# Performance work log

Measured on AMD Instinct MI355X. Metric: run time of the kernel, lower is better.

Reference implementation:

```python
import jax, jax.numpy as jnp
import numpy as np

H = 8
LN_EPS = 1e-5


def _layer_norm(t):
    # LayerNorm over last dim, no affine (elementwise_affine=False, bias=False)
    mu = jnp.mean(t, axis=-1, keepdims=True)
    var = jnp.var(t, axis=-1, keepdims=True)
    return (t - mu) / jnp.sqrt(var + LN_EPS)


def setup_inputs() -> dict:
    key = jax.random.key(0)
    ks = jax.random.split(key, 7)
    B, N, D, K = 2, 8192, 512, 32
    x = jax.random.normal(ks[0], (B, N, D), dtype=jnp.float32)
    idx = jax.random.randint(ks[1], (N, K), 0, N)
    s = 1.0 / np.sqrt(D)  # kaiming-ish init scale for stability
    Wq = jax.random.normal(ks[2], (D, D), dtype=jnp.float32) * s
    Wk = jax.random.normal(ks[3], (D, D), dtype=jnp.float32) * s
    Wv = jax.random.normal(ks[4], (D, D), dtype=jnp.float32) * s
    Wout = jax.random.normal(ks[5], (D, D), dtype=jnp.float32) * s
    bout = jnp.zeros((D,), dtype=jnp.float32)
    return {"x": x, "idx": idx, "Wq": Wq, "Wk": Wk, "Wv": Wv, "Wout": Wout, "bout": bout}


def reference(x, idx, Wq, Wk, Wv, Wout, bout):
    B, N, D = x.shape
    d_k = D // H

    def proj(W):
        # torch Linear: x @ W.T ; reshape to (B, H, N, d_k)
        return (x @ W.T).reshape(B, N, H, d_k).transpose(0, 2, 1, 3)

    Q, K, V = proj(Wq), proj(Wk), proj(Wv)
    # per-head LayerNorm on d_k (all heads identical since no affine params)
    Q = _layer_norm(Q)
    K = _layer_norm(K)

    # grouped (neighborhood) attention: gather K,V at neighbor indices
    Kg = K[:, :, idx]  # (B, H, N, k, d_k)
    Vg = V[:, :, idx]  # (B, H, N, k, d_k)
    scores = jnp.einsum('bhnd,bhnkd->bhnk', Q, Kg) / jnp.sqrt(jnp.asarray(d_k, x.dtype))
    attn = jax.nn.softmax(scores, axis=-1)
    out = jnp.einsum('bhnk,bhnkd->bhnd', attn, Vg)  # (B, H, N, d_k)

    out = out.transpose(0, 2, 1, 3).reshape(B, N, D)
    return out @ Wout.T + bout
```

## Files before the change

### kernel.cpp

```cpp
#include <hip/hip_runtime.h>
#include <hip/hip_bf16.h>
#include <math.h>

#define BB 2
#define NN 8192
#define DD 512
#define HH 8
#define DK 64
#define KNB 32
#define BN (BB*NN)
#define BHN (BB*HH*NN)

typedef __attribute__((ext_vector_type(8))) short bf16x8;
typedef __attribute__((ext_vector_type(8))) unsigned short us8;
typedef __attribute__((ext_vector_type(4))) float f32x4;

__device__ __forceinline__ float bf2f(unsigned short u) {
    return __uint_as_float(((unsigned)u) << 16);
}
__device__ __forceinline__ unsigned short f2bf(float f) {
    return __bfloat16_as_ushort(__float2bfloat16(f));
}

__device__ __forceinline__ void gload_lds16(const void* gptr, void* lptr) {
    __builtin_amdgcn_global_load_lds(
        (const __attribute__((address_space(1))) unsigned int*)gptr,
        (__attribute__((address_space(3))) unsigned int*)lptr,
        16, 0, 0);
}

__global__ __launch_bounds__(256) void cvt_x(const float* __restrict__ in,
                                             unsigned short* __restrict__ out) {
    const int i = (blockIdx.x * 256 + threadIdx.x) * 4;
    const float4 v = *(const float4*)(in + i);
    ushort4 u;
    u.x = f2bf(v.x); u.y = f2bf(v.y); u.z = f2bf(v.z); u.w = f2bf(v.w);
    *(ushort4*)(out + i) = u;
}

__global__ __launch_bounds__(256) void cvt_w(const float* __restrict__ Wq, const float* __restrict__ Wk,
                                             const float* __restrict__ Wv, const float* __restrict__ Wo,
                                             unsigned short* __restrict__ Wfb,
                                             unsigned short* __restrict__ Wob) {
    const int e = (blockIdx.x * 256 + threadIdx.x) * 4;
    const int t = e >> 18;
    const int off = e & 262143;
    const float* src = (t == 0) ? Wq : (t == 1) ? Wk : (t == 2) ? Wv : Wo;
    unsigned short* dst = (t < 3) ? (Wfb + (size_t)t * 262144) : Wob;
    const float4 v = *(const float4*)(src + off);
    ushort4 u;
    u.x = f2bf(v.x); u.y = f2bf(v.y); u.z = f2bf(v.z); u.w = f2bf(v.w);
    *(ushort4*)(dst + off) = u;
}

__global__ __launch_bounds__(256) void gemm_qkv(
    const unsigned short* __restrict__ Xb, const unsigned short* __restrict__ Wfb,
    unsigned short* __restrict__ Qh, unsigned short* __restrict__ Kh,
    unsigned short* __restrict__ Vh)
{
    __shared__ unsigned short Als[128 * 32];
    __shared__ unsigned short Bls[128 * 32];
    const int tid  = threadIdx.x;
    const int wave = tid >> 6, lane = tid & 63;
    const int wm = wave >> 1, wn = wave & 1;
    const int quad = lane >> 4, r = lane & 15;
    const int row0 = blockIdx.x * 128;
    const int c0   = blockIdx.y * 128;

    f32x4 acc[4][4];
    #pragma unroll
    for (int i = 0; i < 4; ++i)
        #pragma unroll
        for (int j = 0; j < 4; ++j) acc[i][j] = (f32x4)0.f;

    const char* Ab = (const char*)Xb;
    const char* Bb = (const char*)Wfb;

    for (int k0 = 0; k0 < 512; k0 += 32) {
        __syncthreads();
        #pragma unroll
        for (int q = 0; q < 2; ++q) {
            const int li = q * 4096 + wave * 1024 + lane * 16;
            const int rr = li >> 6, off = li & 63;
            gload_lds16(Ab + (size_t)(row0 + rr) * 1024 + k0 * 2 + off,
                        (char*)Als + (q * 4096 + wave * 1024));
            gload_lds16(Bb + (size_t)(c0 + rr) * 1024 + k0 * 2 + off,
                        (char*)Bls + (q * 4096 + wave * 1024));
        }
        __syncthreads();

        bf16x8 af[4], bf[4];
        #pragma unroll
        for (int i = 0; i < 4; ++i)
            af[i] = *(const bf16x8*)(&Als[(wm * 64 + i * 16 + r) * 32 + quad * 8]);
        #pragma unroll
        for (int j = 0; j < 4; ++j)
            bf[j] = *(const bf16x8*)(&Bls[(wn * 64 + j * 16 + r) * 32 + quad * 8]);
        #pragma unroll
        for (int i = 0; i < 4; ++i)
            #pragma unroll
            for (int j = 0; j < 4; ++j)
                acc[i][j] = __builtin_amdgcn_mfma_f32_16x16x32_bf16(af[i], bf[j], acc[i][j], 0, 0, 0);
    }

    const int tensor = c0 >> 9;
    unsigned short* OutH = (tensor == 0) ? Qh : (tensor == 1) ? Kh : Vh;

    float mu[4][4], rs[4][4];
    if (tensor < 2) {
        #pragma unroll
        for (int i = 0; i < 4; ++i) {
            #pragma unroll
            for (int reg = 0; reg < 4; ++reg) {
                float sm = acc[i][0][reg] + acc[i][1][reg] + acc[i][2][reg] + acc[i][3][reg];
                sm += __shfl_xor(sm, 1); sm += __shfl_xor(sm, 2);
                sm += __shfl_xor(sm, 4); sm += __shfl_xor(sm, 8);
                const float muv = sm * (1.f / 64.f);
                float qv = 0.f;
                #pragma unroll
                for (int j = 0; j < 4; ++j) {
                    const float dv = acc[i][j][reg] - muv;
                    qv = fmaf(dv, dv, qv);
                }
                qv += __shfl_xor(qv, 1); qv += __shfl_xor(qv, 2);
                qv += __shfl_xor(qv, 4); qv += __shfl_xor(qv, 8);
                mu[i][reg] = muv;
                rs[i][reg] = rsqrtf(qv * (1.f / 64.f) + 1e-5f);
            }
        }
    }

    #pragma unroll
    for (int i = 0; i < 4; ++i) {
        #pragma unroll
        for (int j = 0; j < 4; ++j) {
            const int cc = (c0 & 511) + wn * 64 + j * 16 + r;
            const int h = cc >> 6, d = cc & 63;
            #pragma unroll
            for (int reg = 0; reg < 4; ++reg) {
                const int row = row0 + wm * 64 + i * 16 + quad * 4 + reg;
                const int b = row >> 13, n = row & 8191;
                float v = acc[i][j][reg];
                if (tensor < 2) v = (v - mu[i][reg]) * rs[i][reg];
                OutH[(((size_t)(b * HH + h) * NN + n) << 6) + d] = f2bf(v);
            }
        }
    }
}

__global__ __launch_bounds__(256) void attn(
    const unsigned short* __restrict__ Qh, const unsigned short* __restrict__ Kh,
    const unsigned short* __restrict__ Vh,
    const int* __restrict__ idx, unsigned short* __restrict__ Ob)
{
    const int p = blockIdx.x;
    const int L = ((p & 7) << 12) | (p >> 3);
    const int wid  = L * 4 + (threadIdx.x >> 6);
    const int lane = threadIdx.x & 63;
    const int bh = wid >> 13;
    const int n  = wid & 8191;
    const size_t base = (size_t)bh * NN * DK;

    const int k    = lane >> 1;
    const int half = lane & 1;
    const int g    = idx[n * KNB + k];

    const us8* q8 = (const us8*)(Qh + base + ((size_t)n << 6) + half * 32);
    const us8* k8 = (const us8*)(Kh + base + ((size_t)g << 6) + half * 32);
    float acc = 0.f;
    #pragma unroll
    for (int c = 0; c < 4; ++c) {
        const us8 qa = q8[c], ka = k8[c];
        #pragma unroll
        for (int e = 0; e < 8; ++e)
            acc = fmaf(bf2f(qa[e]), bf2f(ka[e]), acc);
    }
    float s = (acc + __shfl_xor(acc, 1)) * 0.125f;

    float m = s;
    #pragma unroll
    for (int off = 2; off <= 32; off <<= 1) m = fmaxf(m, __shfl_xor(m, off));
    const float e = __expf(s - m);
    float tot = e;
    #pragma unroll
    for (int off = 2; off <= 32; off <<= 1) tot += __shfl_xor(tot, off);
    const float pr = e / tot;

    float o = 0.f;
    #pragma unroll
    for (int kk = 0; kk < 32; ++kk) {
        const int   gk = __builtin_amdgcn_readlane(g, kk * 2);
        const float pk = __uint_as_float(
            __builtin_amdgcn_readlane(__float_as_uint(pr), kk * 2));
        o = fmaf(pk, bf2f(Vh[base + ((size_t)gk << 6) + lane]), o);
    }
    const int b = bh >> 3, h = bh & 7;
    Ob[((size_t)(b * NN + n)) * DD + h * DK + lane] = f2bf(o);
}

__global__ __launch_bounds__(256) void gemm_out(
    const unsigned short* __restrict__ Ob, const unsigned short* __restrict__ Wob,
    const float* __restrict__ bout, float* __restrict__ out)
{
    __shared__ unsigned short Als[128 * 32];
    __shared__ unsigned short Bls[128 * 32];
    const int tid  = threadIdx.x;
    const int wave = tid >> 6, lane = tid & 63;
    const int wm = wave >> 1, wn = wave & 1;
    const int quad = lane >> 4, r = lane & 15;
    const int row0 = blockIdx.x * 128;
    const int c0   = blockIdx.y * 128;

    f32x4 acc[4][4];
    #pragma unroll
    for (int i = 0; i < 4; ++i)
        #pragma unroll
        for (int j = 0; j < 4; ++j) acc[i][j] = (f32x4)0.f;

    const char* Ab = (const char*)Ob;
    const char* Bb = (const char*)Wob;

    for (int k0 = 0; k0 < 512; k0 += 32) {
        __syncthreads();
        #pragma unroll
        for (int q = 0; q < 2; ++q) {
            const int li = q * 4096 + wave * 1024 + lane * 16;
            const int rr = li >> 6, off = li & 63;
            gload_lds16(Ab + (size_t)(row0 + rr) * 1024 + k0 * 2 + off,
                        (char*)Als + (q * 4096 + wave * 1024));
            gload_lds16(Bb + (size_t)(c0 + rr) * 1024 + k0 * 2 + off,
                        (char*)Bls + (q * 4096 + wave * 1024));
        }
        __syncthreads();

        bf16x8 af[4], bf[4];
        #pragma unroll
        for (int i = 0; i < 4; ++i)
            af[i] = *(const bf16x8*)(&Als[(wm * 64 + i * 16 + r) * 32 + quad * 8]);
        #pragma unroll
        for (int j = 0; j < 4; ++j)
            bf[j] = *(const bf16x8*)(&Bls[(wn * 64 + j * 16 + r) * 32 + quad * 8]);
        #pragma unroll
        for (int i = 0; i < 4; ++i)
            #pragma unroll
            for (int j = 0; j < 4; ++j)
                acc[i][j] = __builtin_amdgcn_mfma_f32_16x16x32_bf16(af[i], bf[j], acc[i][j], 0, 0, 0);
    }

    #pragma unroll
    for (int i = 0; i < 4; ++i) {
        #pragma unroll
        for (int j = 0; j < 4; ++j) {
            const int colg = c0 + wn * 64 + j * 16 + r;
            const float bb = bout[colg];
            #pragma unroll
            for (int reg = 0; reg < 4; ++reg) {
                const int row = row0 + wm * 64 + i * 16 + quad * 4 + reg;
                out[((size_t)row << 9) + colg] = acc[i][j][reg] + bb;
            }
        }
    }
}

extern "C" void kernel_launch(void* const* d_in, const int* in_sizes, int n_in,
                              void* d_out, int out_size, void* d_ws, size_t ws_size,
                              hipStream_t stream)
{
    const float* x    = (const float*)d_in[0];
    const int*   idx  = (const int*)  d_in[1];
    const float* Wq   = (const float*)d_in[2];
    const float* Wk   = (const float*)d_in[3];
    const float* Wv   = (const float*)d_in[4];
    const float* Wout = (const float*)d_in[5];
    const float* bout = (const float*)d_in[6];

    char* ws = (char*)d_ws;
    unsigned short* Qh  = (unsigned short*)(ws);
    unsigned short* Kh  = (unsigned short*)(ws + 16777216);
    unsigned short* Vh  = (unsigned short*)(ws + 33554432);
    unsigned short* Xb  = (unsigned short*)(ws + 50331648);
    unsigned short* Ob  = Xb;
    unsigned short* Wfb = (unsigned short*)(ws + 67108864);
    unsigned short* Wob = (unsigned short*)(ws + 68681728);
    float* out = (float*)d_out;

    cvt_x<<<8192, 256, 0, stream>>>(x, Xb);
    cvt_w<<<1024, 256, 0, stream>>>(Wq, Wk, Wv, Wout, Wfb, Wob);

    dim3 g1(BN / 128, 1536 / 128);
    gemm_qkv<<<g1, 256, 0, stream>>>(Xb, Wfb, Qh, Kh, Vh);

    attn<<<BHN / 4, 256, 0, stream>>>(Qh, Kh, Vh, idx, Ob);

    dim3 g2(BN / 128, 512 / 128);
    gemm_out<<<g2, 256, 0, stream>>>(Ob, Wob, bout, out);
}
```

Before: 233.8 us.

## Switch pipeline from bf16 to fp16 with packed dot2 attention and merged conversion

Changes all intermediate storage and MFMA operations from bf16 to fp16. The attention kernel now uses packed fp16 dot2 instructions for the QK dot product and pairs two neighbors per step in the PV accumulation, halving the readlane and FMA work. The two conversion kernels are merged into one launch to save launch overhead. fp16 has a narrower range than bf16, so unnormalized V or x values risk overflow, and probabilities are rounded to fp16.

New measurement: 229.5 us. Within noise of the previous version (-1.8%).

```diff
diff --git a/kernel.cpp b/kernel.cpp
--- a/kernel.cpp
+++ b/kernel.cpp
@@ -11,15 +11,33 @@
 #define BN (BB*NN)
 #define BHN (BB*HH*NN)
 
-typedef __attribute__((ext_vector_type(8))) short bf16x8;
-typedef __attribute__((ext_vector_type(8))) unsigned short us8;
+typedef __attribute__((ext_vector_type(8))) _Float16 f16x8;
+typedef __attribute__((ext_vector_type(2))) _Float16 f16x2;
 typedef __attribute__((ext_vector_type(4))) float f32x4;
 
-__device__ __forceinline__ float bf2f(unsigned short u) {
-    return __uint_as_float(((unsigned)u) << 16);
-}
-__device__ __forceinline__ unsigned short f2bf(float f) {
-    return __bfloat16_as_ushort(__float2bfloat16(f));
+#if __has_builtin(__builtin_amdgcn_fdot2)
+#define HAS_FDOT2 1
+#endif
+
+__device__ __forceinline__ unsigned short f2h(float f) {
+    return __builtin_bit_cast(unsigned short, (_Float16)f);
+}
+__device__ __forceinline__ f16x2 u2h2(unsigned u) {
+    return __builtin_bit_cast(f16x2, u);
+}
+__device__ __forceinline__ float h2f_lo(unsigned u) {
+    return (float)__builtin_bit_cast(_Float16, (unsigned short)(u & 0xffffu));
+}
+__device__ __forceinline__ float h2f_hi(unsigned u) {
+    return (float)__builtin_bit_cast(_Float16, (unsigned short)(u >> 16));
+}
+__device__ __forceinline__ float dot2h(unsigned a, unsigned b, float c) {
+#ifdef HAS_FDOT2
+    return __builtin_amdgcn_fdot2(u2h2(a), u2h2(b), c, false);
+#else
+    c = fmaf(h2f_lo(a), h2f_lo(b), c);
+    return fmaf(h2f_hi(a), h2f_hi(b), c);
+#endif
 }
 
 __device__ __forceinline__ void gload_lds16(const void* gptr, void* lptr) {
@@ -29,27 +47,30 @@
         16, 0, 0);
 }
 
-__global__ __launch_bounds__(256) void cvt_x(const float* __restrict__ in,
-                                             unsigned short* __restrict__ out) {
-    const int i = (blockIdx.x * 256 + threadIdx.x) * 4;
-    const float4 v = *(const float4*)(in + i);
-    ushort4 u;
-    u.x = f2bf(v.x); u.y = f2bf(v.y); u.z = f2bf(v.z); u.w = f2bf(v.w);
-    *(ushort4*)(out + i) = u;
-}
-
-__global__ __launch_bounds__(256) void cvt_w(const float* __restrict__ Wq, const float* __restrict__ Wk,
-                                             const float* __restrict__ Wv, const float* __restrict__ Wo,
-                                             unsigned short* __restrict__ Wfb,
-                                             unsigned short* __restrict__ Wob) {
-    const int e = (blockIdx.x * 256 + threadIdx.x) * 4;
-    const int t = e >> 18;
-    const int off = e & 262143;
-    const float* src = (t == 0) ? Wq : (t == 1) ? Wk : (t == 2) ? Wv : Wo;
-    unsigned short* dst = (t < 3) ? (Wfb + (size_t)t * 262144) : Wob;
+__global__ __launch_bounds__(256) void cvt_all(
+    const float* __restrict__ x,
+    const float* __restrict__ Wq, const float* __restrict__ Wk,
+    const float* __restrict__ Wv, const float* __restrict__ Wo,
+    unsigned short* __restrict__ Xb, unsigned short* __restrict__ Wfb,
+    unsigned short* __restrict__ Wob)
+{
+    const int blk = blockIdx.x;
+    const float* src;
+    unsigned short* dst;
+    int off;
+    if (blk < 8192) {
+        off = (blk * 256 + threadIdx.x) * 4;
+        src = x; dst = Xb;
+    } else {
+        const int e = ((blk - 8192) * 256 + threadIdx.x) * 4;
+        const int t = e >> 18;
+        off = e & 262143;
+        src = (t == 0) ? Wq : (t == 1) ? Wk : (t == 2) ? Wv : Wo;
+        dst = (t < 3) ? (Wfb + (size_t)t * 262144) : Wob;
+    }
     const float4 v = *(const float4*)(src + off);
     ushort4 u;
-    u.x = f2bf(v.x); u.y = f2bf(v.y); u.z = f2bf(v.z); u.w = f2bf(v.w);
+    u.x = f2h(v.x); u.y = f2h(v.y); u.z = f2h(v.z); u.w = f2h(v.w);
     *(ushort4*)(dst + off) = u;
 }
 
@@ -89,18 +110,18 @@
         }
         __syncthreads();
 
-        bf16x8 af[4], bf[4];
+        f16x8 af[4], bf[4];
         #pragma unroll
         for (int i = 0; i < 4; ++i)
-            af[i] = *(const bf16x8*)(&Als[(wm * 64 + i * 16 + r) * 32 + quad * 8]);
+            af[i] = *(const f16x8*)(&Als[(wm * 64 + i * 16 + r) * 32 + quad * 8]);
         #pragma unroll
         for (int j = 0; j < 4; ++j)
-            bf[j] = *(const bf16x8*)(&Bls[(wn * 64 + j * 16 + r) * 32 + quad * 8]);
+            bf[j] = *(const f16x8*)(&Bls[(wn * 64 + j * 16 + r) * 32 + quad * 8]);
         #pragma unroll
         for (int i = 0; i < 4; ++i)
             #pragma unroll
             for (int j = 0; j < 4; ++j)
-                acc[i][j] = __builtin_amdgcn_mfma_f32_16x16x32_bf16(af[i], bf[j], acc[i][j], 0, 0, 0);
+                acc[i][j] = __builtin_amdgcn_mfma_f32_16x16x32_f16(af[i], bf[j], acc[i][j], 0, 0, 0);
     }
 
     const int tensor = c0 >> 9;
@@ -142,7 +163,7 @@
                 const int b = row >> 13, n = row & 8191;
                 float v = acc[i][j][reg];
                 if (tensor < 2) v = (v - mu[i][reg]) * rs[i][reg];
-                OutH[(((size_t)(b * HH + h) * NN + n) << 6) + d] = f2bf(v);
+                OutH[(((size_t)(b * HH + h) * NN + n) << 6) + d] = f2h(v);
             }
         }
     }
@@ -165,15 +186,16 @@
     const int half = lane & 1;
     const int g    = idx[n * KNB + k];
 
-    const us8* q8 = (const us8*)(Qh + base + ((size_t)n << 6) + half * 32);
-    const us8* k8 = (const us8*)(Kh + base + ((size_t)g << 6) + half * 32);
+    const uint4* q4 = (const uint4*)(Qh + base + ((size_t)n << 6) + half * 32);
+    const uint4* k4 = (const uint4*)(Kh + base + ((size_t)g << 6) + half * 32);
     float acc = 0.f;
     #pragma unroll
     for (int c = 0; c < 4; ++c) {
-        const us8 qa = q8[c], ka = k8[c];
-        #pragma unroll
-        for (int e = 0; e < 8; ++e)
-            acc = fmaf(bf2f(qa[e]), bf2f(ka[e]), acc);
+        const uint4 qa = q4[c], ka = k4[c];
+        acc = dot2h(qa.x, ka.x, acc);
+        acc = dot2h(qa.y, ka.y, acc);
+        acc = dot2h(qa.z, ka.z, acc);
+        acc = dot2h(qa.w, ka.w, acc);
     }
     float s = (acc + __shfl_xor(acc, 1)) * 0.125f;
 
@@ -186,16 +208,22 @@
     for (int off = 2; off <= 32; off <<= 1) tot += __shfl_xor(tot, off);
     const float pr = e / tot;
 
+    const unsigned prh = (unsigned)f2h(pr);
+    const unsigned pp = prh | (((unsigned)__shfl_xor((int)prh, 2)) << 16);
+    const unsigned gg = (unsigned)g | (((unsigned)__shfl_xor(g, 2)) << 16);
+
     float o = 0.f;
     #pragma unroll
-    for (int kk = 0; kk < 32; ++kk) {
-        const int   gk = __builtin_amdgcn_readlane(g, kk * 2);
-        const float pk = __uint_as_float(
-            __builtin_amdgcn_readlane(__float_as_uint(pr), kk * 2));
-        o = fmaf(pk, bf2f(Vh[base + ((size_t)gk << 6) + lane]), o);
+    for (int j = 0; j < 16; ++j) {
+        const unsigned gpair = (unsigned)__builtin_amdgcn_readlane((int)gg, j * 4);
+        const unsigned ppair = (unsigned)__builtin_amdgcn_readlane((int)pp, j * 4);
+        const int g0 = (int)(gpair & 0xffffu), g1 = (int)(gpair >> 16);
+        const unsigned v0 = Vh[base + ((size_t)g0 << 6) + lane];
+        const unsigned v1 = Vh[base + ((size_t)g1 << 6) + lane];
+        o = dot2h(v0 | (v1 << 16), ppair, o);
     }
     const int b = bh >> 3, h = bh & 7;
-    Ob[((size_t)(b * NN + n)) * DD + h * DK + lane] = f2bf(o);
+    Ob[((size_t)(b * NN + n)) * DD + h * DK + lane] = f2h(o);
 }
 
 __global__ __launch_bounds__(256) void gemm_out(
@@ -233,18 +261,18 @@
         }
         __syncthreads();
 
-        bf16x8 af[4], bf[4];
+        f16x8 af[4], bf[4];
         #pragma unroll
         for (int i = 0; i < 4; ++i)
-            af[i] = *(const bf16x8*)(&Als[(wm * 64 + i * 16 + r) * 32 + quad * 8]);
+            af[i] = *(const f16x8*)(&Als[(wm * 64 + i * 16 + r) * 32 + quad * 8]);
         #pragma unroll
         for (int j = 0; j < 4; ++j)
-            bf[j] = *(const bf16x8*)(&Bls[(wn * 64 + j * 16 + r) * 32 + quad * 8]);
+            bf[j] = *(const f16x8*)(&Bls[(wn * 64 + j * 16 + r) * 32 + quad * 8]);
         #pragma unroll
         for (int i = 0; i < 4; ++i)
             #pragma unroll
             for (int j = 0; j < 4; ++j)
-                acc[i][j] = __builtin_amdgcn_mfma_f32_16x16x32_bf16(af[i], bf[j], acc[i][j], 0, 0, 0);
+                acc[i][j] = __builtin_amdgcn_mfma_f32_16x16x32_f16(af[i], bf[j], acc[i][j], 0, 0, 0);
     }
 
     #pragma unroll
@@ -284,8 +312,7 @@
     unsigned short* Wob = (unsigned short*)(ws + 68681728);
     float* out = (float*)d_out;
 
-    cvt_x<<<8192, 256, 0, stream>>>(x, Xb);
-    cvt_w<<<1024, 256, 0, stream>>>(Wq, Wk, Wv, Wout, Wfb, Wob);
+    cvt_all<<<9216, 256, 0, stream>>>(x, Wq, Wk, Wv, Wout, Xb, Wfb, Wob);
 
     dim3 g1(BN / 128, 1536 / 128);
     gemm_qkv<<<g1, 256, 0, stream>>>(Xb, Wfb, Qh, Kh, Vh);
```
